# Optimization experiments

Measured on AMD Instinct MI355X. Metric: run time of the kernel, lower is better.

The kernel has to match this reference:

```python
import jax, jax.numpy as jnp
import numpy as np

B, L, E = 4, 2048, 1024
H, DQ, DV = 8, 128, 128
SCALE = 1.0 / np.sqrt(DQ).astype(np.float32)


def setup_inputs() -> dict:
    key = jax.random.key(0)
    ks = jax.random.split(key, 6)
    return {
        "qInputs": jax.random.normal(ks[0], (B, L, E), dtype=jnp.float32),
        "kvInputs": jax.random.normal(ks[1], (B, L, E), dtype=jnp.float32),
        "mask": jnp.zeros((B, H, L, L), dtype=jnp.bool_),
        "W_Q": jax.random.normal(ks[2], (E, H * DQ), dtype=jnp.float32) * 0.02,
        "W_K": jax.random.normal(ks[3], (E, H * DQ), dtype=jnp.float32) * 0.02,
        "W_V": jax.random.normal(ks[4], (E, H * DV), dtype=jnp.float32) * 0.02,
        "W_fc": jax.random.normal(ks[5], (H * DV, E), dtype=jnp.float32) * 0.02,
    }


def reference(qInputs, kvInputs, mask, W_Q, W_K, W_V, W_fc):
    b, lq, _ = qInputs.shape
    lk = kvInputs.shape[1]
    # Projections -> [B, H, L, D]
    Q = (qInputs @ W_Q).reshape(b, lq, H, DQ).transpose(0, 2, 1, 3)
    K = (kvInputs @ W_K).reshape(b, lk, H, DQ).transpose(0, 2, 1, 3)
    V = (kvInputs @ W_V).reshape(b, lk, H, DV).transpose(0, 2, 1, 3)
    # Scaled dot-product with additive mask fill of -1e9
    scores = jnp.einsum("bhqd,bhkd->bhqk", Q, K) * SCALE
    scores = jnp.where(mask, jnp.float32(-1e9), scores)
    attn = jax.nn.softmax(scores, axis=-1)
    ctx = jnp.einsum("bhqk,bhkd->bhqd", attn, V)
    ctx = ctx.transpose(0, 2, 1, 3).reshape(b, lq, H * DV)
    return ctx @ W_fc
```

## Files before the change

### kernel.cpp

```cpp
#include <hip/hip_runtime.h>
#include <stdint.h>

#define LQ 2048
#define EDIM 1024
#define HN 8
#define DH 128
#define BATCH 4
#define SCALE_LOG2E 0.12753785051263942f

typedef short bf16x8 __attribute__((ext_vector_type(8)));
typedef float f32x4 __attribute__((ext_vector_type(4)));
typedef unsigned short u16;
typedef unsigned short u16x4 __attribute__((ext_vector_type(4)));

__device__ __forceinline__ u16 f2bf(float f) {
  union { float f; uint32_t u; } c; c.f = f;
  uint32_t u = c.u;
  return (u16)((u + 0x7fffu + ((u >> 16) & 1u)) >> 16);
}

__device__ __forceinline__ void async16(const void* g, void* l) {
  __builtin_amdgcn_global_load_lds((const __attribute__((address_space(1))) void*)g,
                                   (__attribute__((address_space(3))) void*)l, 16, 0, 0);
}

__device__ __forceinline__ uint32_t lds_b(const u16* p) {
  return (uint32_t)(uintptr_t)(__attribute__((address_space(3))) const u16*)p;
}
__device__ __forceinline__ void ldsr4(bf16x8& d0, bf16x8& d1, bf16x8& d2, bf16x8& d3,
                                      uint32_t a0, uint32_t a1, uint32_t a2, uint32_t a3) {
  asm volatile("ds_read_b128 %0, %4\n\t"
               "ds_read_b128 %1, %5\n\t"
               "ds_read_b128 %2, %6\n\t"
               "ds_read_b128 %3, %7\n\t"
               "s_waitcnt lgkmcnt(0)"
               : "=&v"(d0), "=&v"(d1), "=&v"(d2), "=&v"(d3)
               : "v"(a0), "v"(a1), "v"(a2), "v"(a3));
}
__device__ __forceinline__ uint32_t cvtpk(float lo, float hi) {
  uint32_t r;
  asm("v_cvt_pk_bf16_f32 %0, %1, %2" : "=v"(r) : "v"(lo), "v"(hi));
  return r;
}
__device__ __forceinline__ void bperm8(uint32_t& d0, uint32_t& d1, uint32_t& d2, uint32_t& d3,
                                       uint32_t& d4, uint32_t& d5, uint32_t& d6, uint32_t& d7,
                                       uint32_t al, uint32_t ah,
                                       uint32_t s0, uint32_t s1, uint32_t s2, uint32_t s3) {
  asm volatile("ds_bpermute_b32 %0, %8, %10\n\t"
               "ds_bpermute_b32 %1, %8, %11\n\t"
               "ds_bpermute_b32 %2, %9, %10\n\t"
               "ds_bpermute_b32 %3, %9, %11\n\t"
               "ds_bpermute_b32 %4, %8, %12\n\t"
               "ds_bpermute_b32 %5, %8, %13\n\t"
               "ds_bpermute_b32 %6, %9, %12\n\t"
               "ds_bpermute_b32 %7, %9, %13\n\t"
               "s_waitcnt lgkmcnt(0)"
               : "=&v"(d0), "=&v"(d1), "=&v"(d2), "=&v"(d3),
                 "=&v"(d4), "=&v"(d5), "=&v"(d6), "=&v"(d7)
               : "v"(al), "v"(ah), "v"(s0), "v"(s1), "v"(s2), "v"(s3));
}

__global__ __launch_bounds__(256) void prep_kernel(const float* __restrict__ qIn, const float* __restrict__ kvIn,
                                                   const float* __restrict__ w0, const float* __restrict__ w1,
                                                   const float* __restrict__ w2, const float* __restrict__ w3,
                                                   u16* __restrict__ oq, u16* __restrict__ okv,
                                                   u16* __restrict__ o0, u16* __restrict__ o1,
                                                   u16* __restrict__ o2, u16* __restrict__ o3) {
  __shared__ float tile[32][33];
  const int bid = blockIdx.x;
  const int t = threadIdx.x;
  if (bid < 16384) {
    const float* in = (bid >= 8192) ? kvIn : qIn;
    u16* out = (bid >= 8192) ? okv : oq;
    size_t i = (size_t)(bid & 8191) * 256 + t;
    float4 v = ((const float4*)in)[i];
    u16x4 o;
    o.x = f2bf(v.x); o.y = f2bf(v.y); o.z = f2bf(v.z); o.w = f2bf(v.w);
    ((u16x4*)out)[i] = o;
  } else {
    const int idx = bid - 16384;
    const int z = idx >> 10;
    const int rem = idx & 1023;
    const float* in; u16* out;
    switch (z) {
      case 0: in = w0; out = o0; break;
      case 1: in = w1; out = o1; break;
      case 2: in = w2; out = o2; break;
      default: in = w3; out = o3; break;
    }
    const int tx = t & 31, ty = t >> 5;
    const int x0 = (rem & 31) * 32;
    const int y0 = (rem >> 5) * 32;
#pragma unroll
    for (int j = 0; j < 32; j += 8)
      tile[ty + j][tx] = in[(size_t)(y0 + ty + j) * EDIM + x0 + tx];
    __syncthreads();
#pragma unroll
    for (int j = 0; j < 32; j += 8)
      out[(size_t)(x0 + ty + j) * EDIM + (y0 + tx)] = f2bf(tile[tx][ty + j]);
  }
}

struct GemmCore {
  template <typename EpiF>
  static __device__ __forceinline__ void run(const u16* __restrict__ A, const u16* __restrict__ Bt,
                                             int m0, int n0, u16* As, u16* Bs, EpiF epi) {
    const int tid = threadIdx.x;
    const int l = tid & 63;
    const int w = tid >> 6;
    const int wm = (w >> 1) * 64;
    const int wn = (w & 1) * 64;
    const int fm = l & 15;
    const int q4 = l >> 4;
    const int f7 = fm & 7;
    f32x4 acc[4][4] = {};
    for (int k0 = 0; k0 < EDIM; k0 += 64) {
      __syncthreads();
#pragma unroll
      for (int ii = 0; ii < 4; ++ii) {
        const int rloc = w * 32 + ii * 8 + (l >> 3);
        const int cs = (l & 7) ^ (rloc & 7);
        async16(A + (size_t)(m0 + rloc) * EDIM + k0 + cs * 8, &As[(w * 32 + ii * 8) * 64 + l * 8]);
        async16(Bt + (size_t)(n0 + rloc) * EDIM + k0 + cs * 8, &Bs[(w * 32 + ii * 8) * 64 + l * 8]);
      }
      __syncthreads();
#pragma unroll
      for (int ks = 0; ks < 2; ++ks) {
        const int coff = ((ks * 4 + q4) ^ f7) * 8;
        bf16x8 a[4], b[4];
#pragma unroll
        for (int i = 0; i < 4; ++i) a[i] = *(const bf16x8*)&As[(wm + i * 16 + fm) * 64 + coff];
#pragma unroll
        for (int j = 0; j < 4; ++j) b[j] = *(const bf16x8*)&Bs[(wn + j * 16 + fm) * 64 + coff];
#pragma unroll
        for (int i = 0; i < 4; ++i)
#pragma unroll
          for (int j = 0; j < 4; ++j)
            acc[i][j] = __builtin_amdgcn_mfma_f32_16x16x32_bf16(a[i], b[j], acc[i][j], 0, 0, 0);
      }
    }
    const int rr = q4 * 4;
#pragma unroll
    for (int i = 0; i < 4; ++i)
#pragma unroll
      for (int j = 0; j < 4; ++j)
#pragma unroll
        for (int r = 0; r < 4; ++r)
          epi(m0 + wm + i * 16 + rr + r, n0 + wn + j * 16 + fm, acc[i][j][r]);
  }
};

__global__ __launch_bounds__(256) void qkv_gemm(const u16* __restrict__ xq, const u16* __restrict__ xkv,
                                                const u16* __restrict__ WqT, const u16* __restrict__ WkT,
                                                const u16* __restrict__ WvT,
                                                u16* __restrict__ Qb, u16* __restrict__ Kb,
                                                u16* __restrict__ Vt,
                                                const unsigned char* __restrict__ mask,
                                                unsigned char* __restrict__ flags) {
  __shared__ __align__(16) u16 As[128 * 64];
  __shared__ __align__(16) u16 Bs[128 * 64];
  __shared__ int wany[4];
  const int z = blockIdx.z;
  if (z == 3) {
    const int t = threadIdx.x;
    const int unit0 = (blockIdx.x * 8 + blockIdx.y) * 16;
#pragma unroll 1
    for (int u = 0; u < 16; ++u) {
      const int idx = unit0 + u;
      const int bh = idx >> 8;
      const int tile16 = idx & 255;
      const int qt = tile16 >> 4, kt = tile16 & 15;
      const int r = t >> 1;
      const size_t base = ((size_t)bh * LQ + qt * 128 + r) * LQ + kt * 128 + (t & 1) * 64;
      const uint4* p = (const uint4*)(mask + base);
      uint4 a = p[0], c = p[1], d = p[2], e = p[3];
      uint32_t any = a.x | a.y | a.z | a.w | c.x | c.y | c.z | c.w |
                     d.x | d.y | d.z | d.w | e.x | e.y | e.z | e.w;
      int wa = __any(any != 0);
      if ((t & 63) == 0) wany[t >> 6] = wa;
      __syncthreads();
      if (t == 0)
        flags[(size_t)bh * 256 + tile16] = (unsigned char)(wany[0] | wany[1] | wany[2] | wany[3]);
      __syncthreads();
    }
    return;
  }
  if (z == 0) {
    GemmCore::run(xq, WqT, blockIdx.x * 128, blockIdx.y * 128, As, Bs,
                  [&](int gm, int gn, float v) { Qb[(size_t)gm * EDIM + gn] = f2bf(v); });
  } else if (z == 1) {
    GemmCore::run(xkv, WkT, blockIdx.x * 128, blockIdx.y * 128, As, Bs,
                  [&](int gm, int gn, float v) { Kb[(size_t)gm * EDIM + gn] = f2bf(v); });
  } else {
    GemmCore::run(WvT, xkv, blockIdx.y * 128, blockIdx.x * 128, As, Bs,
                  [&](int gm, int gn, float v) {
                    Vt[((size_t)(gn >> 11) * 1024 + gm) * 2048 + (gn & 2047)] = f2bf(v);
                  });
  }
}

__global__ __launch_bounds__(256) void out_gemm(const u16* __restrict__ ctx, const u16* __restrict__ WfcT,
                                                float* __restrict__ out) {
  __shared__ __align__(16) u16 As[128 * 64];
  __shared__ __align__(16) u16 Bs[128 * 64];
  GemmCore::run(ctx, WfcT, blockIdx.x * 128, blockIdx.y * 128, As, Bs,
                [&](int gm, int gn, float v) { out[(size_t)gm * EDIM + gn] = v; });
}

__global__ __launch_bounds__(256, 2) void attn_kernel(const u16* __restrict__ Qb, const u16* __restrict__ Kb,
                                                      const u16* __restrict__ Vt,
                                                      const unsigned char* __restrict__ mask,
                                                      const unsigned char* __restrict__ flags,
                                                      u16* __restrict__ ctx) {
  __shared__ __align__(16) u16 Ktile[2][64 * 128];
  __shared__ __align__(16) u16 Vtile[2][128 * 64];
  const int tid = threadIdx.x;
  const int l = tid & 63;
  const int w = tid >> 6;
  const int qt = blockIdx.x;
  const int h = blockIdx.y;
  const int b = blockIdx.z;
  const int fm = l & 15;
  const int q4 = l >> 4;
  const int fk = q4 * 8;
  const int f7 = fm & 7;
  const int qbase = qt * 128 + w * 32;
  const int bh = b * HN + h;

  const u16* Kbh = Kb + (size_t)b * LQ * EDIM + h * DH;
  const u16* Vth = Vt + (size_t)bh * DH * LQ;
  const size_t mbase = (size_t)bh * (size_t)LQ * LQ;

  const unsigned char* tf = flags + (size_t)bh * 256 + qt * 16;
  uint32_t fmask = 0;
#pragma unroll
  for (int i = 0; i < 16; ++i) fmask |= (tf[i] ? 1u : 0u) << i;

  bf16x8 qf[2][4];
#pragma unroll
  for (int mt = 0; mt < 2; ++mt)
#pragma unroll
    for (int ks = 0; ks < 4; ++ks)
      qf[mt][ks] = *(const bf16x8*)(Qb + (size_t)(b * LQ + qbase + mt * 16 + fm) * EDIM + h * DH + ks * 32 + fk);

  auto stageK = [&](int kt_, int buf) {
#pragma unroll
    for (int ii = 0; ii < 4; ++ii) {
      const int i = w * 4 + ii;
      const int row = i * 4 + (l >> 4);
      const int g = (l & 15) ^ (row & 7);
      async16(Kbh + (size_t)(kt_ * 64 + row) * EDIM + g * 8, &Ktile[buf][i * 512 + l * 8]);
    }
  };
  auto stageV = [&](int kt_, int buf) {
#pragma unroll
    for (int ii = 0; ii < 4; ++ii) {
      const int i = w * 4 + ii;
      const int row = i * 8 + (l >> 3);
      const int g = (l & 7) ^ (row & 7);
      async16(Vth + (size_t)row * LQ + kt_ * 64 + g * 8, &Vtile[buf][i * 512 + l * 8]);
    }
  };

  stageK(0, 0);
  stageV(0, 0);

  f32x4 o[2][8] = {};
  float lsumv[2] = {0.f, 0.f};
  const uint32_t al = (uint32_t)((fm + 16 * (2 * (q4 & 1))) << 2);
  const uint32_t ah = al + 64u;
  const bool sel_hi = (q4 >> 1) != 0;

  for (int it = 0; it < 32; ++it) {
    const int cur = it & 1;
    __syncthreads();
    if (it + 1 < 32) { stageK(it + 1, 1 - cur); stageV(it + 1, 1 - cur); }

    const u16* KT = &Ktile[cur][0];
    const u16* VT = &Vtile[cur][0];

    f32x4 st[4][2] = {};
#pragma unroll
    for (int ks = 0; ks < 4; ++ks) {
      const int slot = (ks * 4 + q4) ^ f7;
      bf16x8 kf0, kf1, kf2, kf3;
      ldsr4(kf0, kf1, kf2, kf3,
            lds_b(KT + (0 * 16 + fm) * 128 + slot * 8),
            lds_b(KT + (1 * 16 + fm) * 128 + slot * 8),
            lds_b(KT + (2 * 16 + fm) * 128 + slot * 8),
            lds_b(KT + (3 * 16 + fm) * 128 + slot * 8));
#pragma unroll
      for (int mt = 0; mt < 2; ++mt) {
        st[0][mt] = __builtin_amdgcn_mfma_f32_16x16x32_bf16(kf0, qf[mt][ks], st[0][mt], 0, 0, 0);
        st[1][mt] = __builtin_amdgcn_mfma_f32_16x16x32_bf16(kf1, qf[mt][ks], st[1][mt], 0, 0, 0);
        st[2][mt] = __builtin_amdgcn_mfma_f32_16x16x32_bf16(kf2, qf[mt][ks], st[2][mt], 0, 0, 0);
        st[3][mt] = __builtin_amdgcn_mfma_f32_16x16x32_bf16(kf3, qf[mt][ks], st[3][mt], 0, 0, 0);
      }
    }

    const int hasMask = (fmask >> (it >> 1)) & 1;
    uint32_t pk[2][4][2];
#pragma unroll
    for (int mt = 0; mt < 2; ++mt) {
      float sum = 0.f;
      if (hasMask) {
        const unsigned char* mrow = mask + mbase + (size_t)(qbase + mt * 16 + fm) * LQ + it * 64 + q4 * 4;
#pragma unroll
        for (int kt = 0; kt < 4; ++kt) {
          const uint32_t mv = *(const uint32_t*)(mrow + kt * 16);
#pragma unroll
          for (int r = 0; r < 4; ++r) {
            float e = ((mv >> (8 * r)) & 0xffu) ? 0.f : exp2f(st[kt][mt][r] * SCALE_LOG2E);
            st[kt][mt][r] = e;
            sum += e;
          }
        }
      } else {
#pragma unroll
        for (int kt = 0; kt < 4; ++kt)
#pragma unroll
          for (int r = 0; r < 4; ++r) {
            float e = exp2f(st[kt][mt][r] * SCALE_LOG2E);
            st[kt][mt][r] = e;
            sum += e;
          }
      }
      sum += __shfl_xor(sum, 16);
      sum += __shfl_xor(sum, 32);
      lsumv[mt] += sum;
#pragma unroll
      for (int kt = 0; kt < 4; ++kt) {
        pk[mt][kt][0] = cvtpk(st[kt][mt][0], st[kt][mt][1]);
        pk[mt][kt][1] = cvtpk(st[kt][mt][2], st[kt][mt][3]);
      }
    }

#pragma unroll
    for (int ns = 0; ns < 2; ++ns) {
      bf16x8 paf[2];
#pragma unroll
      for (int mt = 0; mt < 2; ++mt) {
        uint32_t t0, t1, t2, t3, u0, u1, u2, u3;
        bperm8(t0, t1, t2, t3, u0, u1, u2, u3, al, ah,
               pk[mt][2 * ns][0], pk[mt][2 * ns][1],
               pk[mt][2 * ns + 1][0], pk[mt][2 * ns + 1][1]);
        union { uint32_t u[4]; bf16x8 v; } fb;
        fb.u[0] = sel_hi ? u0 : t0;
        fb.u[1] = sel_hi ? u1 : t1;
        fb.u[2] = sel_hi ? u2 : t2;
        fb.u[3] = sel_hi ? u3 : t3;
        paf[mt] = fb.v;
      }
      const int vslot = (4 * ns + q4) ^ f7;
      bf16x8 v0, v1, v2, v3, v4, v5, v6, v7;
      ldsr4(v0, v1, v2, v3,
            lds_b(VT + (0 * 16 + fm) * 64 + vslot * 8), lds_b(VT + (1 * 16 + fm) * 64 + vslot * 8),
            lds_b(VT + (2 * 16 + fm) * 64 + vslot * 8), lds_b(VT + (3 * 16 + fm) * 64 + vslot * 8));
      ldsr4(v4, v5, v6, v7,
            lds_b(VT + (4 * 16 + fm) * 64 + vslot * 8), lds_b(VT + (5 * 16 + fm) * 64 + vslot * 8),
            lds_b(VT + (6 * 16 + fm) * 64 + vslot * 8), lds_b(VT + (7 * 16 + fm) * 64 + vslot * 8));
      o[0][0] = __builtin_amdgcn_mfma_f32_16x16x32_bf16(paf[0], v0, o[0][0], 0, 0, 0);
      o[1][0] = __builtin_amdgcn_mfma_f32_16x16x32_bf16(paf[1], v0, o[1][0], 0, 0, 0);
      o[0][1] = __builtin_amdgcn_mfma_f32_16x16x32_bf16(paf[0], v1, o[0][1], 0, 0, 0);
      o[1][1] = __builtin_amdgcn_mfma_f32_16x16x32_bf16(paf[1], v1, o[1][1], 0, 0, 0);
      o[0][2] = __builtin_amdgcn_mfma_f32_16x16x32_bf16(paf[0], v2, o[0][2], 0, 0, 0);
      o[1][2] = __builtin_amdgcn_mfma_f32_16x16x32_bf16(paf[1], v2, o[1][2], 0, 0, 0);
      o[0][3] = __builtin_amdgcn_mfma_f32_16x16x32_bf16(paf[0], v3, o[0][3], 0, 0, 0);
      o[1][3] = __builtin_amdgcn_mfma_f32_16x16x32_bf16(paf[1], v3, o[1][3], 0, 0, 0);
      o[0][4] = __builtin_amdgcn_mfma_f32_16x16x32_bf16(paf[0], v4, o[0][4], 0, 0, 0);
      o[1][4] = __builtin_amdgcn_mfma_f32_16x16x32_bf16(paf[1], v4, o[1][4], 0, 0, 0);
      o[0][5] = __builtin_amdgcn_mfma_f32_16x16x32_bf16(paf[0], v5, o[0][5], 0, 0, 0);
      o[1][5] = __builtin_amdgcn_mfma_f32_16x16x32_bf16(paf[1], v5, o[1][5], 0, 0, 0);
      o[0][6] = __builtin_amdgcn_mfma_f32_16x16x32_bf16(paf[0], v6, o[0][6], 0, 0, 0);
      o[1][6] = __builtin_amdgcn_mfma_f32_16x16x32_bf16(paf[1], v6, o[1][6], 0, 0, 0);
      o[0][7] = __builtin_amdgcn_mfma_f32_16x16x32_bf16(paf[0], v7, o[0][7], 0, 0, 0);
      o[1][7] = __builtin_amdgcn_mfma_f32_16x16x32_bf16(paf[1], v7, o[1][7], 0, 0, 0);
    }
  }

#pragma unroll
  for (int mt = 0; mt < 2; ++mt)
#pragma unroll
    for (int r = 0; r < 4; ++r) {
      float inv = 1.f / __shfl(lsumv[mt], q4 * 4 + r);
      int gq = b * LQ + qbase + mt * 16 + q4 * 4 + r;
#pragma unroll
      for (int dt = 0; dt < 8; ++dt)
        ctx[(size_t)gq * EDIM + h * DH + dt * 16 + fm] = f2bf(o[mt][dt][r] * inv);
    }
}

extern "C" void kernel_launch(void* const* d_in, const int* in_sizes, int n_in,
                              void* d_out, int out_size, void* d_ws, size_t ws_size,
                              hipStream_t stream) {
  const float* qIn = (const float*)d_in[0];
  const float* kvIn = (const float*)d_in[1];
  const unsigned char* mask = (const unsigned char*)d_in[2];
  const float* W_Q = (const float*)d_in[3];
  const float* W_K = (const float*)d_in[4];
  const float* W_V = (const float*)d_in[5];
  const float* W_fc = (const float*)d_in[6];
  float* out = (float*)d_out;

  uint8_t* ws = (uint8_t*)d_ws;
  const size_t MB = 1u << 20;
  u16* xq   = (u16*)(ws);
  u16* xkv  = (u16*)(ws + 16 * MB);
  u16* WqT  = (u16*)(ws + 32 * MB);
  u16* WkT  = (u16*)(ws + 34 * MB);
  u16* WvT  = (u16*)(ws + 36 * MB);
  u16* WfcT = (u16*)(ws + 38 * MB);
  u16* Qb   = (u16*)(ws + 40 * MB);
  u16* Kb   = (u16*)(ws + 56 * MB);
  u16* Vt   = (u16*)(ws + 72 * MB);
  u16* ctx  = (u16*)(ws + 88 * MB);
  unsigned char* flags = (unsigned char*)(ws + 104 * MB);

  prep_kernel<<<20480, 256, 0, stream>>>(qIn, kvIn, W_Q, W_K, W_V, W_fc,
                                         xq, xkv, WqT, WkT, WvT, WfcT);
  qkv_gemm<<<dim3(64, 8, 4), 256, 0, stream>>>(xq, xkv, WqT, WkT, WvT, Qb, Kb, Vt, mask, flags);
  attn_kernel<<<dim3(16, 8, 4), 256, 0, stream>>>(Qb, Kb, Vt, mask, flags, ctx);
  out_gemm<<<dim3(64, 8), 256, 0, stream>>>(ctx, WfcT, out);
}
```

Measured before the change: 846.6 us.

## Software-pipeline LDS reads with MFMAs and fold softmax scale into Q projection

Splits the LDS read and bpermute helpers so the wait is no longer built in. K fragments are double-buffered across the k-steps with partial lgkmcnt waits, and the second half of the V reads is issued before the first PV MFMA block, so LDS latency can overlap matrix math. MFMA blocks are wrapped in s_setprio to favour issuing them. The scale*log2e factor is applied once in the Q projection epilogue instead of per score element before exp2. This raises register pressure (two K fragment buffers and sixteen V fragments live at once) and changes bf16 rounding of Q slightly.

```diff
diff --git a/kernel.cpp b/kernel.cpp
--- a/kernel.cpp
+++ b/kernel.cpp
@@ -27,25 +27,29 @@
 __device__ __forceinline__ uint32_t lds_b(const u16* p) {
   return (uint32_t)(uintptr_t)(__attribute__((address_space(3))) const u16*)p;
 }
-__device__ __forceinline__ void ldsr4(bf16x8& d0, bf16x8& d1, bf16x8& d2, bf16x8& d3,
-                                      uint32_t a0, uint32_t a1, uint32_t a2, uint32_t a3) {
+__device__ __forceinline__ void ldsr4_issue(bf16x8& d0, bf16x8& d1, bf16x8& d2, bf16x8& d3,
+                                            uint32_t a0, uint32_t a1, uint32_t a2, uint32_t a3) {
   asm volatile("ds_read_b128 %0, %4\n\t"
                "ds_read_b128 %1, %5\n\t"
                "ds_read_b128 %2, %6\n\t"
-               "ds_read_b128 %3, %7\n\t"
-               "s_waitcnt lgkmcnt(0)"
+               "ds_read_b128 %3, %7"
                : "=&v"(d0), "=&v"(d1), "=&v"(d2), "=&v"(d3)
                : "v"(a0), "v"(a1), "v"(a2), "v"(a3));
+}
+template <int N>
+__device__ __forceinline__ void lgkm_wait_sb() {
+  asm volatile("s_waitcnt lgkmcnt(%0)" :: "n"(N) : "memory");
+  __builtin_amdgcn_sched_barrier(0);
 }
 __device__ __forceinline__ uint32_t cvtpk(float lo, float hi) {
   uint32_t r;
   asm("v_cvt_pk_bf16_f32 %0, %1, %2" : "=v"(r) : "v"(lo), "v"(hi));
   return r;
 }
-__device__ __forceinline__ void bperm8(uint32_t& d0, uint32_t& d1, uint32_t& d2, uint32_t& d3,
-                                       uint32_t& d4, uint32_t& d5, uint32_t& d6, uint32_t& d7,
-                                       uint32_t al, uint32_t ah,
-                                       uint32_t s0, uint32_t s1, uint32_t s2, uint32_t s3) {
+__device__ __forceinline__ void bperm8_issue(uint32_t& d0, uint32_t& d1, uint32_t& d2, uint32_t& d3,
+                                             uint32_t& d4, uint32_t& d5, uint32_t& d6, uint32_t& d7,
+                                             uint32_t al, uint32_t ah,
+                                             uint32_t s0, uint32_t s1, uint32_t s2, uint32_t s3) {
   asm volatile("ds_bpermute_b32 %0, %8, %10\n\t"
                "ds_bpermute_b32 %1, %8, %11\n\t"
                "ds_bpermute_b32 %2, %9, %10\n\t"
@@ -53,8 +57,7 @@
                "ds_bpermute_b32 %4, %8, %12\n\t"
                "ds_bpermute_b32 %5, %8, %13\n\t"
                "ds_bpermute_b32 %6, %9, %12\n\t"
-               "ds_bpermute_b32 %7, %9, %13\n\t"
-               "s_waitcnt lgkmcnt(0)"
+               "ds_bpermute_b32 %7, %9, %13"
                : "=&v"(d0), "=&v"(d1), "=&v"(d2), "=&v"(d3),
                  "=&v"(d4), "=&v"(d5), "=&v"(d6), "=&v"(d7)
                : "v"(al), "v"(ah), "v"(s0), "v"(s1), "v"(s2), "v"(s3));
@@ -187,7 +190,7 @@
   }
   if (z == 0) {
     GemmCore::run(xq, WqT, blockIdx.x * 128, blockIdx.y * 128, As, Bs,
-                  [&](int gm, int gn, float v) { Qb[(size_t)gm * EDIM + gn] = f2bf(v); });
+                  [&](int gm, int gn, float v) { Qb[(size_t)gm * EDIM + gn] = f2bf(v * SCALE_LOG2E); });
   } else if (z == 1) {
     GemmCore::run(xkv, WkT, blockIdx.x * 128, blockIdx.y * 128, As, Bs,
                   [&](int gm, int gn, float v) { Kb[(size_t)gm * EDIM + gn] = f2bf(v); });
@@ -280,22 +283,38 @@
     const u16* VT = &Vtile[cur][0];
 
     f32x4 st[4][2] = {};
+    bf16x8 kf[2][4];
+    {
+      const int slot = q4 ^ f7;
+      ldsr4_issue(kf[0][0], kf[0][1], kf[0][2], kf[0][3],
+                  lds_b(KT + (0 * 16 + fm) * 128 + slot * 8),
+                  lds_b(KT + (1 * 16 + fm) * 128 + slot * 8),
+                  lds_b(KT + (2 * 16 + fm) * 128 + slot * 8),
+                  lds_b(KT + (3 * 16 + fm) * 128 + slot * 8));
+    }
 #pragma unroll
     for (int ks = 0; ks < 4; ++ks) {
-      const int slot = (ks * 4 + q4) ^ f7;
-      bf16x8 kf0, kf1, kf2, kf3;
-      ldsr4(kf0, kf1, kf2, kf3,
-            lds_b(KT + (0 * 16 + fm) * 128 + slot * 8),
-            lds_b(KT + (1 * 16 + fm) * 128 + slot * 8),
-            lds_b(KT + (2 * 16 + fm) * 128 + slot * 8),
-            lds_b(KT + (3 * 16 + fm) * 128 + slot * 8));
+      const int c = ks & 1;
+      if (ks + 1 < 4) {
+        const int slot = ((ks + 1) * 4 + q4) ^ f7;
+        ldsr4_issue(kf[c ^ 1][0], kf[c ^ 1][1], kf[c ^ 1][2], kf[c ^ 1][3],
+                    lds_b(KT + (0 * 16 + fm) * 128 + slot * 8),
+                    lds_b(KT + (1 * 16 + fm) * 128 + slot * 8),
+                    lds_b(KT + (2 * 16 + fm) * 128 + slot * 8),
+                    lds_b(KT + (3 * 16 + fm) * 128 + slot * 8));
+        lgkm_wait_sb<4>();
+      } else {
+        lgkm_wait_sb<0>();
+      }
+      __builtin_amdgcn_s_setprio(1);
 #pragma unroll
       for (int mt = 0; mt < 2; ++mt) {
-        st[0][mt] = __builtin_amdgcn_mfma_f32_16x16x32_bf16(kf0, qf[mt][ks], st[0][mt], 0, 0, 0);
-        st[1][mt] = __builtin_amdgcn_mfma_f32_16x16x32_bf16(kf1, qf[mt][ks], st[1][mt], 0, 0, 0);
-        st[2][mt] = __builtin_amdgcn_mfma_f32_16x16x32_bf16(kf2, qf[mt][ks], st[2][mt], 0, 0, 0);
-        st[3][mt] = __builtin_amdgcn_mfma_f32_16x16x32_bf16(kf3, qf[mt][ks], st[3][mt], 0, 0, 0);
-      }
+        st[0][mt] = __builtin_amdgcn_mfma_f32_16x16x32_bf16(kf[c][0], qf[mt][ks], st[0][mt], 0, 0, 0);
+        st[1][mt] = __builtin_amdgcn_mfma_f32_16x16x32_bf16(kf[c][1], qf[mt][ks], st[1][mt], 0, 0, 0);
+        st[2][mt] = __builtin_amdgcn_mfma_f32_16x16x32_bf16(kf[c][2], qf[mt][ks], st[2][mt], 0, 0, 0);
+        st[3][mt] = __builtin_amdgcn_mfma_f32_16x16x32_bf16(kf[c][3], qf[mt][ks], st[3][mt], 0, 0, 0);
+      }
+      __builtin_amdgcn_s_setprio(0);
     }
 
     const int hasMask = (fmask >> (it >> 1)) & 1;
@@ -310,7 +329,7 @@
           const uint32_t mv = *(const uint32_t*)(mrow + kt * 16);
 #pragma unroll
           for (int r = 0; r < 4; ++r) {
-            float e = ((mv >> (8 * r)) & 0xffu) ? 0.f : exp2f(st[kt][mt][r] * SCALE_LOG2E);
+            float e = ((mv >> (8 * r)) & 0xffu) ? 0.f : exp2f(st[kt][mt][r]);
             st[kt][mt][r] = e;
             sum += e;
           }
@@ -320,7 +339,7 @@
         for (int kt = 0; kt < 4; ++kt)
 #pragma unroll
           for (int r = 0; r < 4; ++r) {
-            float e = exp2f(st[kt][mt][r] * SCALE_LOG2E);
+            float e = exp2f(st[kt][mt][r]);
             st[kt][mt][r] = e;
             sum += e;
           }
@@ -335,46 +354,90 @@
       }
     }
 
-#pragma unroll
-    for (int ns = 0; ns < 2; ++ns) {
-      bf16x8 paf[2];
-#pragma unroll
-      for (int mt = 0; mt < 2; ++mt) {
-        uint32_t t0, t1, t2, t3, u0, u1, u2, u3;
-        bperm8(t0, t1, t2, t3, u0, u1, u2, u3, al, ah,
-               pk[mt][2 * ns][0], pk[mt][2 * ns][1],
-               pk[mt][2 * ns + 1][0], pk[mt][2 * ns + 1][1]);
+    {
+      bf16x8 v0, v1, v2, v3, v4, v5, v6, v7;
+      const int vs0 = q4 ^ f7;
+      ldsr4_issue(v0, v1, v2, v3,
+                  lds_b(VT + (0 * 16 + fm) * 64 + vs0 * 8), lds_b(VT + (1 * 16 + fm) * 64 + vs0 * 8),
+                  lds_b(VT + (2 * 16 + fm) * 64 + vs0 * 8), lds_b(VT + (3 * 16 + fm) * 64 + vs0 * 8));
+      ldsr4_issue(v4, v5, v6, v7,
+                  lds_b(VT + (4 * 16 + fm) * 64 + vs0 * 8), lds_b(VT + (5 * 16 + fm) * 64 + vs0 * 8),
+                  lds_b(VT + (6 * 16 + fm) * 64 + vs0 * 8), lds_b(VT + (7 * 16 + fm) * 64 + vs0 * 8));
+      uint32_t t0, t1, t2, t3, u0, u1, u2, u3;
+      uint32_t r0, r1, r2, r3, w0, w1, w2, w3;
+      bperm8_issue(t0, t1, t2, t3, u0, u1, u2, u3, al, ah,
+                   pk[0][0][0], pk[0][0][1], pk[0][1][0], pk[0][1][1]);
+      bperm8_issue(r0, r1, r2, r3, w0, w1, w2, w3, al, ah,
+                   pk[1][0][0], pk[1][0][1], pk[1][1][0], pk[1][1][1]);
+      lgkm_wait_sb<0>();
+      bf16x8 paf0, paf1;
+      {
         union { uint32_t u[4]; bf16x8 v; } fb;
-        fb.u[0] = sel_hi ? u0 : t0;
-        fb.u[1] = sel_hi ? u1 : t1;
-        fb.u[2] = sel_hi ? u2 : t2;
-        fb.u[3] = sel_hi ? u3 : t3;
-        paf[mt] = fb.v;
-      }
-      const int vslot = (4 * ns + q4) ^ f7;
-      bf16x8 v0, v1, v2, v3, v4, v5, v6, v7;
-      ldsr4(v0, v1, v2, v3,
-            lds_b(VT + (0 * 16 + fm) * 64 + vslot * 8), lds_b(VT + (1 * 16 + fm) * 64 + vslot * 8),
-            lds_b(VT + (2 * 16 + fm) * 64 + vslot * 8), lds_b(VT + (3 * 16 + fm) * 64 + vslot * 8));
-      ldsr4(v4, v5, v6, v7,
-            lds_b(VT + (4 * 16 + fm) * 64 + vslot * 8), lds_b(VT + (5 * 16 + fm) * 64 + vslot * 8),
-            lds_b(VT + (6 * 16 + fm) * 64 + vslot * 8), lds_b(VT + (7 * 16 + fm) * 64 + vslot * 8));
-      o[0][0] = __builtin_amdgcn_mfma_f32_16x16x32_bf16(paf[0], v0, o[0][0], 0, 0, 0);
-      o[1][0] = __builtin_amdgcn_mfma_f32_16x16x32_bf16(paf[1], v0, o[1][0], 0, 0, 0);
-      o[0][1] = __builtin_amdgcn_mfma_f32_16x16x32_bf16(paf[0], v1, o[0][1], 0, 0, 0);
-      o[1][1] = __builtin_amdgcn_mfma_f32_16x16x32_bf16(paf[1], v1, o[1][1], 0, 0, 0);
-      o[0][2] = __builtin_amdgcn_mfma_f32_16x16x32_bf16(paf[0], v2, o[0][2], 0, 0, 0);
-      o[1][2] = __builtin_amdgcn_mfma_f32_16x16x32_bf16(paf[1], v2, o[1][2], 0, 0, 0);
-      o[0][3] = __builtin_amdgcn_mfma_f32_16x16x32_bf16(paf[0], v3, o[0][3], 0, 0, 0);
-      o[1][3] = __builtin_amdgcn_mfma_f32_16x16x32_bf16(paf[1], v3, o[1][3], 0, 0, 0);
-      o[0][4] = __builtin_amdgcn_mfma_f32_16x16x32_bf16(paf[0], v4, o[0][4], 0, 0, 0);
-      o[1][4] = __builtin_amdgcn_mfma_f32_16x16x32_bf16(paf[1], v4, o[1][4], 0, 0, 0);
-      o[0][5] = __builtin_amdgcn_mfma_f32_16x16x32_bf16(paf[0], v5, o[0][5], 0, 0, 0);
-      o[1][5] = __builtin_amdgcn_mfma_f32_16x16x32_bf16(paf[1], v5, o[1][5], 0, 0, 0);
-      o[0][6] = __builtin_amdgcn_mfma_f32_16x16x32_bf16(paf[0], v6, o[0][6], 0, 0, 0);
-      o[1][6] = __builtin_amdgcn_mfma_f32_16x16x32_bf16(paf[1], v6, o[1][6], 0, 0, 0);
-      o[0][7] = __builtin_amdgcn_mfma_f32_16x16x32_bf16(paf[0], v7, o[0][7], 0, 0, 0);
-      o[1][7] = __builtin_amdgcn_mfma_f32_16x16x32_bf16(paf[1], v7, o[1][7], 0, 0, 0);
+        fb.u[0] = sel_hi ? u0 : t0; fb.u[1] = sel_hi ? u1 : t1;
+        fb.u[2] = sel_hi ? u2 : t2; fb.u[3] = sel_hi ? u3 : t3;
+        paf0 = fb.v;
+        fb.u[0] = sel_hi ? w0 : r0; fb.u[1] = sel_hi ? w1 : r1;
+        fb.u[2] = sel_hi ? w2 : r2; fb.u[3] = sel_hi ? w3 : r3;
+        paf1 = fb.v;
+      }
+      bf16x8 x0, x1, x2, x3, x4, x5, x6, x7;
+      const int vs1 = (4 + q4) ^ f7;
+      ldsr4_issue(x0, x1, x2, x3,
+                  lds_b(VT + (0 * 16 + fm) * 64 + vs1 * 8), lds_b(VT + (1 * 16 + fm) * 64 + vs1 * 8),
+                  lds_b(VT + (2 * 16 + fm) * 64 + vs1 * 8), lds_b(VT + (3 * 16 + fm) * 64 + vs1 * 8));
+      ldsr4_issue(x4, x5, x6, x7,
+                  lds_b(VT + (4 * 16 + fm) * 64 + vs1 * 8), lds_b(VT + (5 * 16 + fm) * 64 + vs1 * 8),
+                  lds_b(VT + (6 * 16 + fm) * 64 + vs1 * 8), lds_b(VT + (7 * 16 + fm) * 64 + vs1 * 8));
+      __builtin_amdgcn_s_setprio(1);
+      o[0][0] = __builtin_amdgcn_mfma_f32_16x16x32_bf16(paf0, v0, o[0][0], 0, 0, 0);
+      o[1][0] = __builtin_amdgcn_mfma_f32_16x16x32_bf16(paf1, v0, o[1][0], 0, 0, 0);
+      o[0][1] = __builtin_amdgcn_mfma_f32_16x16x32_bf16(paf0, v1, o[0][1], 0, 0, 0);
+      o[1][1] = __builtin_amdgcn_mfma_f32_16x16x32_bf16(paf1, v1, o[1][1], 0, 0, 0);
+      o[0][2] = __builtin_amdgcn_mfma_f32_16x16x32_bf16(paf0, v2, o[0][2], 0, 0, 0);
+      o[1][2] = __builtin_amdgcn_mfma_f32_16x16x32_bf16(paf1, v2, o[1][2], 0, 0, 0);
+      o[0][3] = __builtin_amdgcn_mfma_f32_16x16x32_bf16(paf0, v3, o[0][3], 0, 0, 0);
+      o[1][3] = __builtin_amdgcn_mfma_f32_16x16x32_bf16(paf1, v3, o[1][3], 0, 0, 0);
+      o[0][4] = __builtin_amdgcn_mfma_f32_16x16x32_bf16(paf0, v4, o[0][4], 0, 0, 0);
+      o[1][4] = __builtin_amdgcn_mfma_f32_16x16x32_bf16(paf1, v4, o[1][4], 0, 0, 0);
+      o[0][5] = __builtin_amdgcn_mfma_f32_16x16x32_bf16(paf0, v5, o[0][5], 0, 0, 0);
+      o[1][5] = __builtin_amdgcn_mfma_f32_16x16x32_bf16(paf1, v5, o[1][5], 0, 0, 0);
+      o[0][6] = __builtin_amdgcn_mfma_f32_16x16x32_bf16(paf0, v6, o[0][6], 0, 0, 0);
+      o[1][6] = __builtin_amdgcn_mfma_f32_16x16x32_bf16(paf1, v6, o[1][6], 0, 0, 0);
+      o[0][7] = __builtin_amdgcn_mfma_f32_16x16x32_bf16(paf0, v7, o[0][7], 0, 0, 0);
+      o[1][7] = __builtin_amdgcn_mfma_f32_16x16x32_bf16(paf1, v7, o[1][7], 0, 0, 0);
+      __builtin_amdgcn_s_setprio(0);
+      bperm8_issue(t0, t1, t2, t3, u0, u1, u2, u3, al, ah,
+                   pk[0][2][0], pk[0][2][1], pk[0][3][0], pk[0][3][1]);
+      bperm8_issue(r0, r1, r2, r3, w0, w1, w2, w3, al, ah,
+                   pk[1][2][0], pk[1][2][1], pk[1][3][0], pk[1][3][1]);
+      lgkm_wait_sb<0>();
+      {
+        union { uint32_t u[4]; bf16x8 v; } fb;
+        fb.u[0] = sel_hi ? u0 : t0; fb.u[1] = sel_hi ? u1 : t1;
+        fb.u[2] = sel_hi ? u2 : t2; fb.u[3] = sel_hi ? u3 : t3;
+        paf0 = fb.v;
+        fb.u[0] = sel_hi ? w0 : r0; fb.u[1] = sel_hi ? w1 : r1;
+        fb.u[2] = sel_hi ? w2 : r2; fb.u[3] = sel_hi ? w3 : r3;
+        paf1 = fb.v;
+      }
+      __builtin_amdgcn_s_setprio(1);
+      o[0][0] = __builtin_amdgcn_mfma_f32_16x16x32_bf16(paf0, x0, o[0][0], 0, 0, 0);
+      o[1][0] = __builtin_amdgcn_mfma_f32_16x16x32_bf16(paf1, x0, o[1][0], 0, 0, 0);
+      o[0][1] = __builtin_amdgcn_mfma_f32_16x16x32_bf16(paf0, x1, o[0][1], 0, 0, 0);
+      o[1][1] = __builtin_amdgcn_mfma_f32_16x16x32_bf16(paf1, x1, o[1][1], 0, 0, 0);
+      o[0][2] = __builtin_amdgcn_mfma_f32_16x16x32_bf16(paf0, x2, o[0][2], 0, 0, 0);
+      o[1][2] = __builtin_amdgcn_mfma_f32_16x16x32_bf16(paf1, x2, o[1][2], 0, 0, 0);
+      o[0][3] = __builtin_amdgcn_mfma_f32_16x16x32_bf16(paf0, x3, o[0][3], 0, 0, 0);
+      o[1][3] = __builtin_amdgcn_mfma_f32_16x16x32_bf16(paf1, x3, o[1][3], 0, 0, 0);
+      o[0][4] = __builtin_amdgcn_mfma_f32_16x16x32_bf16(paf0, x4, o[0][4], 0, 0, 0);
+      o[1][4] = __builtin_amdgcn_mfma_f32_16x16x32_bf16(paf1, x4, o[1][4], 0, 0, 0);
+      o[0][5] = __builtin_amdgcn_mfma_f32_16x16x32_bf16(paf0, x5, o[0][5], 0, 0, 0);
+      o[1][5] = __builtin_amdgcn_mfma_f32_16x16x32_bf16(paf1, x5, o[1][5], 0, 0, 0);
+      o[0][6] = __builtin_amdgcn_mfma_f32_16x16x32_bf16(paf0, x6, o[0][6], 0, 0, 0);
+      o[1][6] = __builtin_amdgcn_mfma_f32_16x16x32_bf16(paf1, x6, o[1][6], 0, 0, 0);
+      o[0][7] = __builtin_amdgcn_mfma_f32_16x16x32_bf16(paf0, x7, o[0][7], 0, 0, 0);
+      o[1][7] = __builtin_amdgcn_mfma_f32_16x16x32_bf16(paf1, x7, o[1][7], 0, 0, 0);
+      __builtin_amdgcn_s_setprio(0);
     }
   }
 
```

After: 848.4 us. No clear change (+0.2%).
